# Kernel optimization log

Hardware: AMD Instinct MI355X
Metric: run time of the kernel (lower is better)

Reference implementation:

```python
import math
import jax, jax.numpy as jnp
import numpy as np

FS = 96000.0
N_BIQUADS = 16
HPF_FREQ_RANGE = (20.0, 500.0)
LPF_FREQ_RANGE = (5000.0, 20000.0)
SHELF_FREQ_RANGE = (50.0, 16000.0)
PEAK_FREQ_RANGE = (100.0, 15000.0)
Q_RANGE = (0.5, 16.0)
GAIN_RANGE = (-24.0, 24.0)
BROADBAND_RANGE = (-60.0, 0.0)


def _denorm_log(norm, lo, hi):
    return jnp.exp(math.log(lo) + norm * (math.log(hi) - math.log(lo)))


def _coef_highpass(fc, Q):
    w0 = 2.0 * math.pi * fc / FS
    alpha = jnp.sin(w0) / (2.0 * Q)
    c = jnp.cos(w0)
    b0 = (1 + c) / 2; b1 = -(1 + c); b2 = (1 + c) / 2
    a0 = 1 + alpha; a1 = -2 * c; a2 = 1 - alpha
    return b0 / a0, b1 / a0, b2 / a0, a1 / a0, a2 / a0


def _coef_lowpass(fc, Q):
    w0 = 2.0 * math.pi * fc / FS
    alpha = jnp.sin(w0) / (2.0 * Q)
    c = jnp.cos(w0)
    b0 = (1 - c) / 2; b1 = 1 - c; b2 = (1 - c) / 2
    a0 = 1 + alpha; a1 = -2 * c; a2 = 1 - alpha
    return b0 / a0, b1 / a0, b2 / a0, a1 / a0, a2 / a0


def _coef_lowshelf(fc, gain_db, Q):
    A = 10.0 ** (gain_db / 40.0)
    w0 = 2.0 * math.pi * fc / FS
    alpha = jnp.sin(w0) / (2.0 * Q)
    c = jnp.cos(w0)
    sA = jnp.sqrt(A)
    b0 = A * (A + 1 - (A - 1) * c + 2 * sA * alpha)
    b1 = 2 * A * (A - 1 - (A + 1) * c)
    b2 = A * (A + 1 - (A - 1) * c - 2 * sA * alpha)
    a0 = A + 1 + (A - 1) * c + 2 * sA * alpha
    a1 = -2 * (A - 1 + (A + 1) * c)
    a2 = A + 1 + (A - 1) * c - 2 * sA * alpha
    return b0 / a0, b1 / a0, b2 / a0, a1 / a0, a2 / a0


def _coef_highshelf(fc, gain_db, Q):
    A = 10.0 ** (gain_db / 40.0)
    w0 = 2.0 * math.pi * fc / FS
    alpha = jnp.sin(w0) / (2.0 * Q)
    c = jnp.cos(w0)
    sA = jnp.sqrt(A)
    b0 = A * (A + 1 + (A - 1) * c + 2 * sA * alpha)
    b1 = -2 * A * (A - 1 + (A + 1) * c)
    b2 = A * (A + 1 + (A - 1) * c - 2 * sA * alpha)
    a0 = A + 1 - (A - 1) * c + 2 * sA * alpha
    a1 = 2 * (A - 1 - (A + 1) * c)
    a2 = A + 1 - (A - 1) * c - 2 * sA * alpha
    return b0 / a0, b1 / a0, b2 / a0, a1 / a0, a2 / a0


def _coef_peak(fc, gain_db, Q):
    A = 10.0 ** (gain_db / 40.0)
    w0 = 2.0 * math.pi * fc / FS
    alpha = jnp.sin(w0) / (2.0 * Q)
    c = jnp.cos(w0)
    b0 = 1 + alpha * A; b1 = -2 * c; b2 = 1 - alpha * A
    a0 = 1 + alpha / A; a1 = -2 * c; a2 = 1 - alpha / A
    return b0 / a0, b1 / a0, b2 / a0, a1 / a0, a2 / a0


def _biquad(x, coefs):
    # x: (B, T); coefs: 5 arrays of shape (B,)
    b0, b1, b2, a1, a2 = coefs

    def step(carry, xt):  # xt: (B,)
        s1, s2 = carry
        y = b0 * xt + s1
        return (b1 * xt - a1 * y + s2, b2 * xt - a2 * y), y

    z = jnp.zeros(x.shape[0], x.dtype)
    _, ys = jax.lax.scan(step, (z, z), x.T)  # ys: (T, B)
    return ys.T


def _chain(audio, params):
    B = audio.shape[0]
    bp = params[:, :N_BIQUADS * 3].reshape(B, N_BIQUADS, 3)
    bb_lo, bb_hi = BROADBAND_RANGE
    in_db = bb_lo + params[:, -2] * (bb_hi - bb_lo)
    out_db = bb_lo + params[:, -1] * (bb_hi - bb_lo)
    x = audio * (10.0 ** (in_db / 20.0))[:, None]

    for i in range(N_BIQUADS):
        fn, gn, qn = bp[:, i, 0], bp[:, i, 1], bp[:, i, 2]
        Q = _denorm_log(qn, *Q_RANGE)
        gain = GAIN_RANGE[0] + gn * (GAIN_RANGE[1] - GAIN_RANGE[0])
        if i == 0:  # HPF
            coefs = _coef_highpass(_denorm_log(fn, *HPF_FREQ_RANGE), Q)
        elif i == 15:  # LPF
            coefs = _coef_lowpass(_denorm_log(fn, *LPF_FREQ_RANGE), Q)
        elif i == 1:  # low shelf
            coefs = _coef_lowshelf(_denorm_log(fn, *SHELF_FREQ_RANGE), gain, Q)
        elif i == 14:  # high shelf
            coefs = _coef_highshelf(_denorm_log(fn, *SHELF_FREQ_RANGE), gain, Q)
        else:  # peaking EQ
            coefs = _coef_peak(_denorm_log(fn, *PEAK_FREQ_RANGE), gain, Q)
        x = _biquad(x, coefs)

    return x * (10.0 ** (out_db / 20.0))[:, None]


def setup_inputs() -> dict:
    key = jax.random.key(0)
    k1, k2 = jax.random.split(key)
    audio = jax.random.normal(k1, (16, 262144), dtype=jnp.float32)
    params = jax.random.uniform(k2, (16, 50), dtype=jnp.float32)
    return {"audio": audio, "params": params}


def reference(audio, params):
    return _chain(audio, params)
```

## Files before the change

kernel.cpp:

```cpp
#include <hip/hip_runtime.h>
#include <math.h>

#define BATCH   16
#define T_LEN   262144
#define NB      16
#define L       64
#define GRP     64
#define NG      64
#define NCHUNK  4096

#define DPI 3.14159265358979323846264338327950288

#define OFF_COEF  0
#define OFF_AL    1536
#define OFF_AG    17920
#define OFF_QEND  34304
#define OFF_SARR  67072
#define OFF_P     102400

__device__ inline void stage_coefs(int i, double fn, double gn, double qn,
                                   double& B0, double& B1, double& B2,
                                   double& A1, double& A2) {
    const double FS = 96000.0;
    double Q    = exp(log(0.5) + qn * (log(16.0) - log(0.5)));
    double gain = -24.0 + gn * 48.0;
    double lo, hi;
    if (i == 0)            { lo = 20.0;   hi = 500.0;   }
    else if (i == 15)      { lo = 5000.0; hi = 20000.0; }
    else if (i == 1 || i == 14) { lo = 50.0; hi = 16000.0; }
    else                   { lo = 100.0;  hi = 15000.0; }
    double fc    = exp(log(lo) + fn * (log(hi) - log(lo)));
    double w0    = 2.0 * DPI * fc / FS;
    double alpha = sin(w0) / (2.0 * Q);
    double c     = cos(w0);
    double b0, b1, b2, a0, a1, a2;
    if (i == 0) {
        b0 = (1.0 + c) * 0.5; b1 = -(1.0 + c); b2 = (1.0 + c) * 0.5;
        a0 = 1.0 + alpha; a1 = -2.0 * c; a2 = 1.0 - alpha;
    } else if (i == 15) {
        b0 = (1.0 - c) * 0.5; b1 = 1.0 - c; b2 = (1.0 - c) * 0.5;
        a0 = 1.0 + alpha; a1 = -2.0 * c; a2 = 1.0 - alpha;
    } else if (i == 1) {
        double A = pow(10.0, gain / 40.0), sA = sqrt(A);
        b0 = A * ((A + 1.0) - (A - 1.0) * c + 2.0 * sA * alpha);
        b1 = 2.0 * A * ((A - 1.0) - (A + 1.0) * c);
        b2 = A * ((A + 1.0) - (A - 1.0) * c - 2.0 * sA * alpha);
        a0 = (A + 1.0) + (A - 1.0) * c + 2.0 * sA * alpha;
        a1 = -2.0 * ((A - 1.0) + (A + 1.0) * c);
        a2 = (A + 1.0) + (A - 1.0) * c - 2.0 * sA * alpha;
    } else if (i == 14) {
        double A = pow(10.0, gain / 40.0), sA = sqrt(A);
        b0 = A * ((A + 1.0) + (A - 1.0) * c + 2.0 * sA * alpha);
        b1 = -2.0 * A * ((A - 1.0) + (A + 1.0) * c);
        b2 = A * ((A + 1.0) + (A - 1.0) * c - 2.0 * sA * alpha);
        a0 = (A + 1.0) - (A - 1.0) * c + 2.0 * sA * alpha;
        a1 = 2.0 * ((A - 1.0) - (A + 1.0) * c);
        a2 = (A + 1.0) - (A - 1.0) * c - 2.0 * sA * alpha;
    } else {
        double A = pow(10.0, gain / 40.0);
        b0 = 1.0 + alpha * A; b1 = -2.0 * c; b2 = 1.0 - alpha * A;
        a0 = 1.0 + alpha / A; a1 = -2.0 * c; a2 = 1.0 - alpha / A;
    }
    B0 = b0 / a0; B1 = b1 / a0; B2 = b2 / a0; A1 = a1 / a0; A2 = a2 / a0;
}

__global__ __launch_bounds__(256) void k0_setup(const float* __restrict__ params,
                                                float* __restrict__ coefs,
                                                float* __restrict__ AL,
                                                float* __restrict__ AG) {
    int b = blockIdx.x;
    int t = threadIdx.x;
    __shared__ double cf[NB][5];
    __shared__ double M1[32 * 32];
    __shared__ double M2[32 * 32];

    if (t < NB) {
        double B0, B1, B2, A1, A2;
        stage_coefs(t, (double)params[b * 50 + t * 3 + 0],
                       (double)params[b * 50 + t * 3 + 1],
                       (double)params[b * 50 + t * 3 + 2], B0, B1, B2, A1, A2);
        float f0 = (float)B0, f1 = (float)B1, f2 = (float)B2, f3 = (float)A1, f4 = (float)A2;
        cf[t][0] = (double)f0; cf[t][1] = (double)f1; cf[t][2] = (double)f2;
        cf[t][3] = (double)f3; cf[t][4] = (double)f4;
        float* cp = coefs + b * 96 + t * 5;
        cp[0] = f0; cp[1] = f1; cp[2] = f2; cp[3] = f3; cp[4] = f4;
    }
    if (t == NB) {
        double indb = -60.0 + (double)params[b * 50 + 48] * 60.0;
        coefs[b * 96 + 80] = (float)pow(10.0, indb / 20.0);
    }
    if (t == NB + 1) {
        double outdb = -60.0 + (double)params[b * 50 + 49] * 60.0;
        coefs[b * 96 + 81] = (float)pow(10.0, outdb / 20.0);
    }
    __syncthreads();

    if (t < 32) {
        double s1[NB], s2[NB];
#pragma unroll
        for (int i = 0; i < NB; i++) {
            s1[i] = (t == 2 * i) ? 1.0 : 0.0;
            s2[i] = (t == 2 * i + 1) ? 1.0 : 0.0;
        }
        double u = 0.0;
#pragma unroll
        for (int i = 0; i < NB; i++) {
            double y  = cf[i][0] * u + s1[i];
            double n1 = cf[i][1] * u - cf[i][3] * y + s2[i];
            double n2 = cf[i][2] * u - cf[i][4] * y;
            s1[i] = n1; s2[i] = n2; u = y;
        }
#pragma unroll
        for (int i = 0; i < NB; i++) {
            M1[(2 * i) * 32 + t]     = s1[i];
            M1[(2 * i + 1) * 32 + t] = s2[i];
        }
    }
    __syncthreads();

    int c  = t & 31;
    int r0 = t >> 5;
    double* src = M1;
    double* dst = M2;
    for (int sq = 0; sq < 12; sq++) {
        double acc[4] = {0.0, 0.0, 0.0, 0.0};
        for (int k = 0; k < 32; k++) {
            double bv = src[k * 32 + c];
#pragma unroll
            for (int e = 0; e < 4; e++)
                acc[e] += src[(e * 8 + r0) * 32 + k] * bv;
        }
#pragma unroll
        for (int e = 0; e < 4; e++) dst[(e * 8 + r0) * 32 + c] = acc[e];
        __syncthreads();
        { double* tmp = src; src = dst; dst = tmp; }
        if (sq == 5) {
#pragma unroll
            for (int e = 0; e < 4; e++) {
                int idx = (e * 8 + r0) * 32 + c;
                AL[b * 1024 + idx] = (float)src[idx];
            }
        }
        if (sq == 11) {
#pragma unroll
            for (int e = 0; e < 4; e++) {
                int idx = (e * 8 + r0) * 32 + c;
                AG[b * 1024 + idx] = (float)src[idx];
            }
        }
        __syncthreads();
    }
}


__global__ __launch_bounds__(64, 1) void k1_pass1(const float* __restrict__ audio,
                                                  const float* __restrict__ coefs,
                                                  const float* __restrict__ AL,
                                                  float* __restrict__ P,
                                                  float* __restrict__ Qend) {
    int blk   = blockIdx.x;
    int batch = blk >> 6;
    int grp   = blk & 63;
    int lane  = threadIdx.x;
    int chunk = grp * GRP + lane;

    const float4* xp = (const float4*)(audio + (size_t)batch * T_LEN + (size_t)chunk * L);
    float4 xbuf[16];
#pragma unroll
    for (int tt = 0; tt < 16; tt++) xbuf[tt] = xp[tt];

    const float* cf = coefs + batch * 96;
    float c0[NB], c1[NB], c2[NB], c3[NB], c4[NB];
#pragma unroll
    for (int i = 0; i < NB; i++) {
        c0[i] = cf[i * 5 + 0]; c1[i] = cf[i * 5 + 1]; c2[i] = cf[i * 5 + 2];
        c3[i] = cf[i * 5 + 3]; c4[i] = cf[i * 5 + 4];
    }
    float ing = cf[80];

    float s1[NB], s2[NB];
#pragma unroll
    for (int i = 0; i < NB; i++) { s1[i] = 0.f; s2[i] = 0.f; }

#pragma unroll
    for (int tt = 0; tt < 16; tt++) {
        float xs[4] = {xbuf[tt].x, xbuf[tt].y, xbuf[tt].z, xbuf[tt].w};
#pragma unroll
        for (int j = 0; j < 4; j++) {
            float u = ing * xs[j];
#pragma unroll
            for (int i = 0; i < NB; i++) {
                float y  = fmaf(c0[i], u, s1[i]);
                float n1 = fmaf(c1[i], u, s2[i]); n1 = fmaf(-c3[i], y, n1);
                float n2 = c2[i] * u;             n2 = fmaf(-c4[i], y, n2);
                s1[i] = n1; s2[i] = n2; u = y;
            }
        }
    }

    __shared__ float plds[GRP][33];
    float* pp = P + ((size_t)(batch * NCHUNK + chunk)) * 32;
#pragma unroll
    for (int i = 0; i < NB; i++) {
        float2 v; v.x = s1[i]; v.y = s2[i];
        *(float2*)(pp + 2 * i) = v;
        plds[lane][2 * i]     = s1[i];
        plds[lane][2 * i + 1] = s2[i];
    }
    __syncthreads();

    int row  = lane & 31;
    int half = lane >> 5;
    const float* alr = AL + batch * 1024 + row * 32 + half * 16;
    float ar[16];
#pragma unroll
    for (int j = 0; j < 16; j++) ar[j] = alr[j];
    float q = 0.f;
    for (int k = 0; k < GRP; k++) {
        float acc = (half == 0) ? plds[k][row] : 0.f;
#pragma unroll
        for (int j = 0; j < 16; j++)
            acc = fmaf(ar[j], __shfl(q, half * 16 + j, 64), acc);
        acc += __shfl_xor(acc, 32, 64);
        q = acc;
    }
    if (lane < 32) Qend[(batch * NG + grp) * 32 + row] = q;
}

__global__ __launch_bounds__(64, 1) void k2_combine(const float* __restrict__ AG,
                                                    const float* __restrict__ Qend,
                                                    float* __restrict__ Sarr) {
    int batch = blockIdx.x;
    int lane  = threadIdx.x;
    int row   = lane & 31;
    int half  = lane >> 5;

    __shared__ float qe[NG][32];
    __shared__ float ss[NG][32];

    const float4* qsrc = (const float4*)(Qend + (size_t)batch * NG * 32);
    float4* qdst = (float4*)&qe[0][0];
    for (int i = lane; i < NG * 32 / 4; i += 64) qdst[i] = qsrc[i];

    const float* agr = AG + batch * 1024 + row * 32 + half * 16;
    float ar[16];
#pragma unroll
    for (int j = 0; j < 16; j++) ar[j] = agr[j];
    __syncthreads();

    float S = 0.f;
    for (int g = 0; g < NG; g++) {
        if (half == 0) ss[g][row] = S;
        float acc = (half == 0) ? qe[g][row] : 0.f;
#pragma unroll
        for (int j = 0; j < 16; j++)
            acc = fmaf(ar[j], __shfl(S, half * 16 + j, 64), acc);
        acc += __shfl_xor(acc, 32, 64);
        S = acc;
    }
    __syncthreads();

    const float4* s4 = (const float4*)&ss[0][0];
    float4* sd = (float4*)(Sarr + (size_t)batch * NG * 32);
    for (int i = lane; i < NG * 32 / 4; i += 64) sd[i] = s4[i];
}

__global__ __launch_bounds__(64, 1) void k3_pass2(const float* __restrict__ audio,
                                                  const float* __restrict__ coefs,
                                                  const float* __restrict__ AL,
                                                  const float* __restrict__ P,
                                                  const float* __restrict__ Sarr,
                                                  float* __restrict__ out) {
    int blk   = blockIdx.x;
    int batch = blk >> 6;
    int grp   = blk & 63;
    int lane  = threadIdx.x;
    int chunk = grp * GRP + lane;

    const float4* xp = (const float4*)(audio + (size_t)batch * T_LEN + (size_t)chunk * L);
    float4 xbuf[16];
#pragma unroll
    for (int tt = 0; tt < 16; tt++) xbuf[tt] = xp[tt];

    __shared__ float plds[GRP][33];
    __shared__ float slds[GRP][33];

    const float4* pp4 = (const float4*)(P + ((size_t)(batch * NCHUNK + chunk)) * 32);
#pragma unroll
    for (int r4 = 0; r4 < 8; r4++) {
        float4 v = pp4[r4];
        plds[lane][4 * r4 + 0] = v.x;
        plds[lane][4 * r4 + 1] = v.y;
        plds[lane][4 * r4 + 2] = v.z;
        plds[lane][4 * r4 + 3] = v.w;
    }
    __syncthreads();

    {
        int row  = lane & 31;
        int half = lane >> 5;
        const float* alr = AL + batch * 1024 + row * 32 + half * 16;
        float ar[16];
#pragma unroll
        for (int j = 0; j < 16; j++) ar[j] = alr[j];
        float q = Sarr[(batch * NG + grp) * 32 + row];
        for (int k = 0; k < GRP; k++) {
            if (half == 0) slds[k][row] = q;
            float acc = (half == 0) ? plds[k][row] : 0.f;
#pragma unroll
            for (int j = 0; j < 16; j++)
                acc = fmaf(ar[j], __shfl(q, half * 16 + j, 64), acc);
            acc += __shfl_xor(acc, 32, 64);
            q = acc;
        }
    }
    __syncthreads();

    const float* cf = coefs + batch * 96;
    float c0[NB], c1[NB], c2[NB], c3[NB], c4[NB];
#pragma unroll
    for (int i = 0; i < NB; i++) {
        c0[i] = cf[i * 5 + 0]; c1[i] = cf[i * 5 + 1]; c2[i] = cf[i * 5 + 2];
        c3[i] = cf[i * 5 + 3]; c4[i] = cf[i * 5 + 4];
    }
    float ing  = cf[80];
    float outg = cf[81];

    float s1[NB], s2[NB];
#pragma unroll
    for (int i = 0; i < NB; i++) {
        s1[i] = slds[lane][2 * i];
        s2[i] = slds[lane][2 * i + 1];
    }

    float4* yp = (float4*)(out + (size_t)batch * T_LEN + (size_t)chunk * L);
#pragma unroll
    for (int tt = 0; tt < 16; tt++) {
        float xs[4] = {xbuf[tt].x, xbuf[tt].y, xbuf[tt].z, xbuf[tt].w};
        float ys[4];
#pragma unroll
        for (int j = 0; j < 4; j++) {
            float u = ing * xs[j];
#pragma unroll
            for (int i = 0; i < NB; i++) {
                float y  = fmaf(c0[i], u, s1[i]);
                float n1 = fmaf(c1[i], u, s2[i]); n1 = fmaf(-c3[i], y, n1);
                float n2 = c2[i] * u;             n2 = fmaf(-c4[i], y, n2);
                s1[i] = n1; s2[i] = n2; u = y;
            }
            ys[j] = outg * u;
        }
        float4 yv; yv.x = ys[0]; yv.y = ys[1]; yv.z = ys[2]; yv.w = ys[3];
        yp[tt] = yv;
    }
}

extern "C" void kernel_launch(void* const* d_in, const int* in_sizes, int n_in,
                              void* d_out, int out_size, void* d_ws, size_t ws_size,
                              hipStream_t stream) {
    const float* audio  = (const float*)d_in[0];
    const float* params = (const float*)d_in[1];
    float* out = (float*)d_out;
    float* ws  = (float*)d_ws;

    float* coefs = ws + OFF_COEF;
    float* AL    = ws + OFF_AL;
    float* AG    = ws + OFF_AG;
    float* Qend  = ws + OFF_QEND;
    float* Sarr  = ws + OFF_SARR;
    float* P     = ws + OFF_P;

    k0_setup<<<BATCH, 256, 0, stream>>>(params, coefs, AL, AG);
    k1_pass1<<<BATCH * NG, 64, 0, stream>>>(audio, coefs, AL, P, Qend);
    k2_combine<<<BATCH, 64, 0, stream>>>(AG, Qend, Sarr);
    k3_pass2<<<BATCH * NG, 64, 0, stream>>>(audio, coefs, AL, P, Sarr, out);
}
```

Measured before the change: 161.2 us.

## Split intra-block scan into 4 chains and add hierarchical three-level state combine

```diff
diff --git a/kernel.cpp b/kernel.cpp
--- a/kernel.cpp
+++ b/kernel.cpp
@@ -6,17 +6,24 @@
 #define NB      16
 #define L       64
 #define GRP     64
+#define SUB     16
+#define CHAINS  4
+#define NSUB    256
+#define NSUP    16
 #define NG      64
 #define NCHUNK  4096
 
 #define DPI 3.14159265358979323846264338327950288
 
-#define OFF_COEF  0
-#define OFF_AL    1536
-#define OFF_AG    17920
-#define OFF_QEND  34304
-#define OFF_SARR  67072
-#define OFF_P     102400
+#define OFF_COEF   0
+#define OFF_A64    1536
+#define OFF_A1K    17920
+#define OFF_A16K   34304
+#define OFF_QEND   50688
+#define OFF_QSUP   181760
+#define OFF_SSUP   189952
+#define OFF_SARR   198144
+#define OFF_P      329216
 
 __device__ inline void stage_coefs(int i, double fn, double gn, double qn,
                                    double& B0, double& B1, double& B2,
@@ -66,8 +73,9 @@
 
 __global__ __launch_bounds__(256) void k0_setup(const float* __restrict__ params,
                                                 float* __restrict__ coefs,
-                                                float* __restrict__ AL,
-                                                float* __restrict__ AG) {
+                                                float* __restrict__ A64,
+                                                float* __restrict__ A1K,
+                                                float* __restrict__ A16K) {
     int b = blockIdx.x;
     int t = threadIdx.x;
     __shared__ double cf[NB][5];
@@ -122,7 +130,7 @@
     int r0 = t >> 5;
     double* src = M1;
     double* dst = M2;
-    for (int sq = 0; sq < 12; sq++) {
+    for (int sq = 0; sq < 14; sq++) {
         double acc[4] = {0.0, 0.0, 0.0, 0.0};
         for (int k = 0; k < 32; k++) {
             double bv = src[k * 32 + c];
@@ -134,28 +142,21 @@
         for (int e = 0; e < 4; e++) dst[(e * 8 + r0) * 32 + c] = acc[e];
         __syncthreads();
         { double* tmp = src; src = dst; dst = tmp; }
-        if (sq == 5) {
+        float* out_m = (sq == 5) ? A64 : (sq == 9) ? A1K : (sq == 13) ? A16K : nullptr;
+        if (out_m) {
 #pragma unroll
             for (int e = 0; e < 4; e++) {
                 int idx = (e * 8 + r0) * 32 + c;
-                AL[b * 1024 + idx] = (float)src[idx];
+                out_m[b * 1024 + idx] = (float)src[idx];
             }
         }
-        if (sq == 11) {
-#pragma unroll
-            for (int e = 0; e < 4; e++) {
-                int idx = (e * 8 + r0) * 32 + c;
-                AG[b * 1024 + idx] = (float)src[idx];
-            }
-        }
         __syncthreads();
     }
 }
-
 
 __global__ __launch_bounds__(64, 1) void k1_pass1(const float* __restrict__ audio,
                                                   const float* __restrict__ coefs,
-                                                  const float* __restrict__ AL,
+                                                  const float* __restrict__ A64,
                                                   float* __restrict__ P,
                                                   float* __restrict__ Qend) {
     int blk   = blockIdx.x;
@@ -164,11 +165,6 @@
     int lane  = threadIdx.x;
     int chunk = grp * GRP + lane;
 
-    const float4* xp = (const float4*)(audio + (size_t)batch * T_LEN + (size_t)chunk * L);
-    float4 xbuf[16];
-#pragma unroll
-    for (int tt = 0; tt < 16; tt++) xbuf[tt] = xp[tt];
-
     const float* cf = coefs + batch * 96;
     float c0[NB], c1[NB], c2[NB], c3[NB], c4[NB];
 #pragma unroll
@@ -182,9 +178,13 @@
 #pragma unroll
     for (int i = 0; i < NB; i++) { s1[i] = 0.f; s2[i] = 0.f; }
 
-#pragma unroll
+    const float4* xp = (const float4*)(audio + (size_t)batch * T_LEN + (size_t)chunk * L);
+    float4 cur = xp[0];
+    float4 nxt = xp[1];
+#pragma unroll 1
     for (int tt = 0; tt < 16; tt++) {
-        float xs[4] = {xbuf[tt].x, xbuf[tt].y, xbuf[tt].z, xbuf[tt].w};
+        float4 fut = xp[(tt < 14) ? (tt + 2) : 15];
+        float xs[4] = {cur.x, cur.y, cur.z, cur.w};
 #pragma unroll
         for (int j = 0; j < 4; j++) {
             float u = ing * xs[j];
@@ -196,6 +196,7 @@
                 s1[i] = n1; s2[i] = n2; u = y;
             }
         }
+        cur = nxt; nxt = fut;
     }
 
     __shared__ float plds[GRP][33];
@@ -211,63 +212,137 @@
 
     int row  = lane & 31;
     int half = lane >> 5;
-    const float* alr = AL + batch * 1024 + row * 32 + half * 16;
+    const float* alr = A64 + batch * 1024 + row * 32 + half * 16;
     float ar[16];
 #pragma unroll
     for (int j = 0; j < 16; j++) ar[j] = alr[j];
+    float q0 = 0.f, q1 = 0.f, q2 = 0.f, q3 = 0.f;
+#pragma unroll 1
+    for (int j = 0; j < SUB; j++) {
+        float a0 = (half == 0) ? plds[0 * SUB + j][row] : 0.f;
+        float a1 = (half == 0) ? plds[1 * SUB + j][row] : 0.f;
+        float a2 = (half == 0) ? plds[2 * SUB + j][row] : 0.f;
+        float a3 = (half == 0) ? plds[3 * SUB + j][row] : 0.f;
+#pragma unroll
+        for (int t = 0; t < 16; t++) {
+            float w = ar[t];
+            int src = half * 16 + t;
+            a0 = fmaf(w, __shfl(q0, src, 64), a0);
+            a1 = fmaf(w, __shfl(q1, src, 64), a1);
+            a2 = fmaf(w, __shfl(q2, src, 64), a2);
+            a3 = fmaf(w, __shfl(q3, src, 64), a3);
+        }
+        a0 += __shfl_xor(a0, 32, 64);
+        a1 += __shfl_xor(a1, 32, 64);
+        a2 += __shfl_xor(a2, 32, 64);
+        a3 += __shfl_xor(a3, 32, 64);
+        q0 = a0; q1 = a1; q2 = a2; q3 = a3;
+    }
+    if (lane < 32) {
+        float* qe = Qend + ((size_t)(batch * NSUB + grp * CHAINS)) * 32 + row;
+        qe[0 * 32] = q0; qe[1 * 32] = q1; qe[2 * 32] = q2; qe[3 * 32] = q3;
+    }
+}
+
+__global__ __launch_bounds__(64, 1) void k2a(const float* __restrict__ A1K,
+                                             const float* __restrict__ Qend,
+                                             float* __restrict__ Qsup) {
+    int batch = blockIdx.x >> 4;
+    int sup   = blockIdx.x & 15;
+    int lane  = threadIdx.x;
+    int row   = lane & 31;
+    int half  = lane >> 5;
+
+    float pv[16];
+#pragma unroll
+    for (int j = 0; j < 16; j++)
+        pv[j] = (half == 0) ? Qend[((size_t)(batch * NSUB + sup * 16 + j)) * 32 + row] : 0.f;
+
+    const float* agr = A1K + batch * 1024 + row * 32 + half * 16;
+    float ar[16];
+#pragma unroll
+    for (int j = 0; j < 16; j++) ar[j] = agr[j];
+
     float q = 0.f;
-    for (int k = 0; k < GRP; k++) {
-        float acc = (half == 0) ? plds[k][row] : 0.f;
-#pragma unroll
-        for (int j = 0; j < 16; j++)
-            acc = fmaf(ar[j], __shfl(q, half * 16 + j, 64), acc);
+#pragma unroll 1
+    for (int j = 0; j < 16; j++) {
+        float acc = pv[j];
+#pragma unroll
+        for (int t = 0; t < 16; t++)
+            acc = fmaf(ar[t], __shfl(q, half * 16 + t, 64), acc);
         acc += __shfl_xor(acc, 32, 64);
         q = acc;
     }
-    if (lane < 32) Qend[(batch * NG + grp) * 32 + row] = q;
-}
-
-__global__ __launch_bounds__(64, 1) void k2_combine(const float* __restrict__ AG,
-                                                    const float* __restrict__ Qend,
-                                                    float* __restrict__ Sarr) {
+    if (lane < 32) Qsup[((size_t)(batch * NSUP + sup)) * 32 + row] = q;
+}
+
+__global__ __launch_bounds__(64, 1) void k2b(const float* __restrict__ A16K,
+                                             const float* __restrict__ Qsup,
+                                             float* __restrict__ Ssup) {
     int batch = blockIdx.x;
     int lane  = threadIdx.x;
     int row   = lane & 31;
     int half  = lane >> 5;
 
-    __shared__ float qe[NG][32];
-    __shared__ float ss[NG][32];
-
-    const float4* qsrc = (const float4*)(Qend + (size_t)batch * NG * 32);
-    float4* qdst = (float4*)&qe[0][0];
-    for (int i = lane; i < NG * 32 / 4; i += 64) qdst[i] = qsrc[i];
-
-    const float* agr = AG + batch * 1024 + row * 32 + half * 16;
+    float pv[16];
+#pragma unroll
+    for (int j = 0; j < 16; j++)
+        pv[j] = (half == 0) ? Qsup[((size_t)(batch * NSUP + j)) * 32 + row] : 0.f;
+
+    const float* agr = A16K + batch * 1024 + row * 32 + half * 16;
     float ar[16];
 #pragma unroll
     for (int j = 0; j < 16; j++) ar[j] = agr[j];
-    __syncthreads();
 
     float S = 0.f;
-    for (int g = 0; g < NG; g++) {
-        if (half == 0) ss[g][row] = S;
-        float acc = (half == 0) ? qe[g][row] : 0.f;
-#pragma unroll
-        for (int j = 0; j < 16; j++)
-            acc = fmaf(ar[j], __shfl(S, half * 16 + j, 64), acc);
+#pragma unroll 1
+    for (int s = 0; s < 16; s++) {
+        if (lane < 32) Ssup[((size_t)(batch * NSUP + s)) * 32 + row] = S;
+        float acc = pv[s];
+#pragma unroll
+        for (int t = 0; t < 16; t++)
+            acc = fmaf(ar[t], __shfl(S, half * 16 + t, 64), acc);
         acc += __shfl_xor(acc, 32, 64);
         S = acc;
     }
-    __syncthreads();
-
-    const float4* s4 = (const float4*)&ss[0][0];
-    float4* sd = (float4*)(Sarr + (size_t)batch * NG * 32);
-    for (int i = lane; i < NG * 32 / 4; i += 64) sd[i] = s4[i];
+}
+
+__global__ __launch_bounds__(64, 1) void k2c(const float* __restrict__ A1K,
+                                             const float* __restrict__ Qend,
+                                             const float* __restrict__ Ssup,
+                                             float* __restrict__ Sarr) {
+    int batch = blockIdx.x >> 4;
+    int sup   = blockIdx.x & 15;
+    int lane  = threadIdx.x;
+    int row   = lane & 31;
+    int half  = lane >> 5;
+
+    float pv[16];
+#pragma unroll
+    for (int j = 0; j < 16; j++)
+        pv[j] = (half == 0) ? Qend[((size_t)(batch * NSUB + sup * 16 + j)) * 32 + row] : 0.f;
+
+    const float* agr = A1K + batch * 1024 + row * 32 + half * 16;
+    float ar[16];
+#pragma unroll
+    for (int j = 0; j < 16; j++) ar[j] = agr[j];
+
+    float q = Ssup[((size_t)(batch * NSUP + sup)) * 32 + row];
+#pragma unroll 1
+    for (int j = 0; j < 16; j++) {
+        if (lane < 32) Sarr[((size_t)(batch * NSUB + sup * 16 + j)) * 32 + row] = q;
+        float acc = pv[j];
+#pragma unroll
+        for (int t = 0; t < 16; t++)
+            acc = fmaf(ar[t], __shfl(q, half * 16 + t, 64), acc);
+        acc += __shfl_xor(acc, 32, 64);
+        q = acc;
+    }
 }
 
 __global__ __launch_bounds__(64, 1) void k3_pass2(const float* __restrict__ audio,
                                                   const float* __restrict__ coefs,
-                                                  const float* __restrict__ AL,
+                                                  const float* __restrict__ A64,
                                                   const float* __restrict__ P,
                                                   const float* __restrict__ Sarr,
                                                   float* __restrict__ out) {
@@ -277,13 +352,7 @@
     int lane  = threadIdx.x;
     int chunk = grp * GRP + lane;
 
-    const float4* xp = (const float4*)(audio + (size_t)batch * T_LEN + (size_t)chunk * L);
-    float4 xbuf[16];
-#pragma unroll
-    for (int tt = 0; tt < 16; tt++) xbuf[tt] = xp[tt];
-
     __shared__ float plds[GRP][33];
-    __shared__ float slds[GRP][33];
 
     const float4* pp4 = (const float4*)(P + ((size_t)(batch * NCHUNK + chunk)) * 32);
 #pragma unroll
@@ -299,19 +368,38 @@
     {
         int row  = lane & 31;
         int half = lane >> 5;
-        const float* alr = AL + batch * 1024 + row * 32 + half * 16;
+        const float* alr = A64 + batch * 1024 + row * 32 + half * 16;
         float ar[16];
 #pragma unroll
         for (int j = 0; j < 16; j++) ar[j] = alr[j];
-        float q = Sarr[(batch * NG + grp) * 32 + row];
-        for (int k = 0; k < GRP; k++) {
-            if (half == 0) slds[k][row] = q;
-            float acc = (half == 0) ? plds[k][row] : 0.f;
-#pragma unroll
-            for (int j = 0; j < 16; j++)
-                acc = fmaf(ar[j], __shfl(q, half * 16 + j, 64), acc);
-            acc += __shfl_xor(acc, 32, 64);
-            q = acc;
+        const float* sp = Sarr + ((size_t)(batch * NSUB + grp * CHAINS)) * 32 + row;
+        float q0 = sp[0 * 32], q1 = sp[1 * 32], q2 = sp[2 * 32], q3 = sp[3 * 32];
+#pragma unroll 1
+        for (int j = 0; j < SUB; j++) {
+            float a0 = (half == 0) ? plds[0 * SUB + j][row] : 0.f;
+            float a1 = (half == 0) ? plds[1 * SUB + j][row] : 0.f;
+            float a2 = (half == 0) ? plds[2 * SUB + j][row] : 0.f;
+            float a3 = (half == 0) ? plds[3 * SUB + j][row] : 0.f;
+            if (half == 0) {
+                plds[0 * SUB + j][row] = q0;
+                plds[1 * SUB + j][row] = q1;
+                plds[2 * SUB + j][row] = q2;
+                plds[3 * SUB + j][row] = q3;
+            }
+#pragma unroll
+            for (int t = 0; t < 16; t++) {
+                float w = ar[t];
+                int src = half * 16 + t;
+                a0 = fmaf(w, __shfl(q0, src, 64), a0);
+                a1 = fmaf(w, __shfl(q1, src, 64), a1);
+                a2 = fmaf(w, __shfl(q2, src, 64), a2);
+                a3 = fmaf(w, __shfl(q3, src, 64), a3);
+            }
+            a0 += __shfl_xor(a0, 32, 64);
+            a1 += __shfl_xor(a1, 32, 64);
+            a2 += __shfl_xor(a2, 32, 64);
+            a3 += __shfl_xor(a3, 32, 64);
+            q0 = a0; q1 = a1; q2 = a2; q3 = a3;
         }
     }
     __syncthreads();
@@ -329,14 +417,18 @@
     float s1[NB], s2[NB];
 #pragma unroll
     for (int i = 0; i < NB; i++) {
-        s1[i] = slds[lane][2 * i];
-        s2[i] = slds[lane][2 * i + 1];
-    }
-
+        s1[i] = plds[lane][2 * i];
+        s2[i] = plds[lane][2 * i + 1];
+    }
+
+    const float4* xp = (const float4*)(audio + (size_t)batch * T_LEN + (size_t)chunk * L);
     float4* yp = (float4*)(out + (size_t)batch * T_LEN + (size_t)chunk * L);
-#pragma unroll
+    float4 cur = xp[0];
+    float4 nxt = xp[1];
+#pragma unroll 1
     for (int tt = 0; tt < 16; tt++) {
-        float xs[4] = {xbuf[tt].x, xbuf[tt].y, xbuf[tt].z, xbuf[tt].w};
+        float4 fut = xp[(tt < 14) ? (tt + 2) : 15];
+        float xs[4] = {cur.x, cur.y, cur.z, cur.w};
         float ys[4];
 #pragma unroll
         for (int j = 0; j < 4; j++) {
@@ -352,6 +444,7 @@
         }
         float4 yv; yv.x = ys[0]; yv.y = ys[1]; yv.z = ys[2]; yv.w = ys[3];
         yp[tt] = yv;
+        cur = nxt; nxt = fut;
     }
 }
 
@@ -364,14 +457,19 @@
     float* ws  = (float*)d_ws;
 
     float* coefs = ws + OFF_COEF;
-    float* AL    = ws + OFF_AL;
-    float* AG    = ws + OFF_AG;
+    float* A64   = ws + OFF_A64;
+    float* A1K   = ws + OFF_A1K;
+    float* A16K  = ws + OFF_A16K;
     float* Qend  = ws + OFF_QEND;
+    float* Qsup  = ws + OFF_QSUP;
+    float* Ssup  = ws + OFF_SSUP;
     float* Sarr  = ws + OFF_SARR;
     float* P     = ws + OFF_P;
 
-    k0_setup<<<BATCH, 256, 0, stream>>>(params, coefs, AL, AG);
-    k1_pass1<<<BATCH * NG, 64, 0, stream>>>(audio, coefs, AL, P, Qend);
-    k2_combine<<<BATCH, 64, 0, stream>>>(AG, Qend, Sarr);
-    k3_pass2<<<BATCH * NG, 64, 0, stream>>>(audio, coefs, AL, P, Sarr, out);
-}
+    k0_setup<<<BATCH, 256, 0, stream>>>(params, coefs, A64, A1K, A16K);
+    k1_pass1<<<BATCH * NG, 64, 0, stream>>>(audio, coefs, A64, P, Qend);
+    k2a<<<BATCH * NSUP, 64, 0, stream>>>(A1K, Qend, Qsup);
+    k2b<<<BATCH, 64, 0, stream>>>(A16K, Qsup, Ssup);
+    k2c<<<BATCH * NSUP, 64, 0, stream>>>(A1K, Qend, Ssup, Sarr);
+    k3_pass2<<<BATCH * NG, 64, 0, stream>>>(audio, coefs, A64, P, Sarr, out);
+}
```

Result: no change. 159.5 us (-1.0%).
